# Kernel optimization log

Hardware: AMD Instinct MI355X
Metric: run time of the kernel (lower is better)

The kernel has to match this reference:

```python
import jax, jax.numpy as jnp
import numpy as np

N_E = 4096
E_DIM = 64
BETA = 0.25


def setup_inputs() -> dict:
    key = jax.random.key(0)
    k1, k2 = jax.random.split(key)
    z = jax.random.normal(k1, (16, E_DIM, 32, 32), dtype=jnp.float32)
    embedding = jax.random.normal(k2, (N_E, E_DIM), dtype=jnp.float32)
    return {"z": z, "embedding": embedding}


def reference(z, embedding):
    # b c h w -> b h w c
    zc = jnp.transpose(z, (0, 2, 3, 1))  # [B,H,W,C]
    B, H, W, C = zc.shape
    zf = zc.reshape(-1, C)  # [N, C]

    # Squared Euclidean distances (argmin is identical to cdist p=2 argmin)
    # d2[n,e] = |z|^2 - 2 z.e + |e|^2
    d2 = (
        jnp.sum(zf * zf, axis=1, keepdims=True)
        - 2.0 * (zf @ embedding.T)
        + jnp.sum(embedding * embedding, axis=1)[None, :]
    )  # [N, n_e]
    idx = jnp.argmin(d2, axis=1)  # [N]

    z_q = embedding[idx].reshape(B, H, W, C)

    # dist_p == 2 losses
    loss_d1 = jnp.mean((jax.lax.stop_gradient(z_q) - zc) ** 2)
    loss_d2 = jnp.mean((z_q - jax.lax.stop_gradient(zc)) ** 2)
    loss = BETA * loss_d1 + loss_d2

    # Straight-through estimator
    z_q = zc + jax.lax.stop_gradient(z_q - zc)

    indices = idx.reshape(B, H, W)
    z_q = jnp.transpose(z_q, (0, 3, 1, 2))  # b h w c -> b c h w
    return z_q, loss, indices
```

## Files before the change

kernel.cpp:

```cpp
#include <hip/hip_runtime.h>

typedef float f32x4 __attribute__((ext_vector_type(4)));
typedef short bf16x8 __attribute__((ext_vector_type(8)));

#define HW_ 1024
#define NE_ 4096
#define CHW_ 65536
#define ZQ_SIZE 1048576
#define LOSS_OFF ZQ_SIZE
#define IDX_OFF (ZQ_SIZE + 1)
#define LOSS_SCALE (1.25f / 1048576.f)
#define EPS_GAP 0.1f

union FragU { unsigned u[4]; bf16x8 v; };

__device__ __forceinline__ unsigned umin_(unsigned a, unsigned b) { return a < b ? a : b; }
__device__ __forceinline__ unsigned umax_(unsigned a, unsigned b) { return a > b ? a : b; }

__device__ __forceinline__ void top2_(unsigned key, unsigned& s1, unsigned& s2) {
    unsigned t;
    asm("v_med3_u32 %0, %1, %2, %3" : "=v"(t) : "v"(key), "v"(s1), "v"(s2));
    s2 = t;
    s1 = umin_(s1, key);
}

__device__ __forceinline__ void split8(const float* v, FragU& hi, FragU& lo) {
#pragma unroll
    for (int p = 0; p < 4; p++) {
        float a = v[2 * p], b = v[2 * p + 1];
        unsigned ua = __float_as_uint(a), ub = __float_as_uint(b);
        hi.u[p] = (ua >> 16) | (ub & 0xFFFF0000u);
        float la = a - __uint_as_float(ua & 0xFFFF0000u);
        float lb = b - __uint_as_float(ub & 0xFFFF0000u);
        lo.u[p] = (__float_as_uint(la) >> 16) | (__float_as_uint(lb) & 0xFFFF0000u);
    }
}

__device__ __forceinline__ void gload_lds16(const void* g, void* l) {
    __builtin_amdgcn_global_load_lds(
        (const __attribute__((address_space(1))) unsigned*)g,
        (__attribute__((address_space(3))) unsigned*)l, 16, 0, 0);
}

__global__ __launch_bounds__(256) void vq_pre(
        const float* __restrict__ z, const float* __restrict__ emb,
        float* __restrict__ h_e, float* __restrict__ h_z,
        char* __restrict__ zfrag, char* __restrict__ efrag,
        float* __restrict__ out) {
    const int bid = blockIdx.x, tid = threadIdx.x;
    if (bid < 512) {
        __shared__ float red[2][2][16];
        int u = bid * 256 + tid;
        int l = u & 63, s = (u >> 6) & 1, t = u >> 7;
        int n = t * 16 + (l & 15);
        int b = n >> 10, hw = n & 1023;
        int c0 = s * 32 + (l >> 4) * 8;
        const float* zp = z + (size_t)b * CHW_ + hw;
        float v[8];
        float ss = 0.f;
#pragma unroll
        for (int j = 0; j < 8; j++) {
            v[j] = zp[(c0 + j) * HW_];
            ss = fmaf(v[j], v[j], ss);
        }
        FragU hi, lo;
        split8(v, hi, lo);
        char* base = zfrag + (size_t)t * 4096 + l * 16;
        *(FragU*)(base + s * 1024) = hi;
        *(FragU*)(base + (2 + s) * 1024) = lo;
        ss += __shfl_xor(ss, 16);
        ss += __shfl_xor(ss, 32);
        if ((l >> 4) == 0) red[tid >> 7][s][l & 15] = ss;
        __syncthreads();
        if (tid < 32) {
            int tt = tid >> 4, r = tid & 15;
            h_z[(bid * 2 + tt) * 16 + r] = 0.5f * (red[tt][0][r] + red[tt][1][r]);
        }
    } else if (bid < 640) {
        int u = (bid - 512) * 256 + tid;
        int l = u & 63, s = (u >> 6) & 1, t = u >> 7;
        int er = t * 16 + (l & 15);
        int c0 = s * 32 + (l >> 4) * 8;
        const float* ep = emb + (size_t)er * 64 + c0;
        float4 ea = *(const float4*)(ep);
        float4 eb = *(const float4*)(ep + 4);
        float v[8];
        v[0] = -ea.x; v[1] = -ea.y; v[2] = -ea.z; v[3] = -ea.w;
        v[4] = -eb.x; v[5] = -eb.y; v[6] = -eb.z; v[7] = -eb.w;
        FragU hi, lo;
        split8(v, hi, lo);
        char* base = efrag + (size_t)t * 4096 + l * 16;
        *(FragU*)(base + s * 1024) = hi;
        *(FragU*)(base + (2 + s) * 1024) = lo;
    } else {
        int t = (bid - 640) * 256 + tid;
        const float4* er = (const float4*)(emb + (size_t)t * 64);
        float s = 0.f;
#pragma unroll
        for (int k = 0; k < 16; k++) {
            float4 e4 = er[k];
            s = fmaf(e4.x, e4.x, s); s = fmaf(e4.y, e4.y, s);
            s = fmaf(e4.z, e4.z, s); s = fmaf(e4.w, e4.w, s);
        }
        h_e[t] = 0.5f * s;
        if (t == 0) out[LOSS_OFF] = 0.f;
    }
}

__global__ __launch_bounds__(512) void vq_mfma(
        const char* __restrict__ zfrag, const char* __restrict__ efrag,
        const float* __restrict__ h_e, const float* __restrict__ h_z,
        unsigned* __restrict__ k1q, unsigned* __restrict__ k2q) {
    __shared__ char buf[2][32768];
    __shared__ __attribute__((aligned(16))) float sh_he[512];

    const int tid = threadIdx.x;
    const int lane = tid & 63;
    const int w = tid >> 6;
    const int lrow = lane & 15;
    const int lgrp = lane >> 4;
    const int es = blockIdx.x >> 5;
    const int rb = blockIdx.x & 31;
    const int e0t = es * 32;
    const int rt0 = rb * 32 + w * 4;

    sh_he[tid] = h_e[es * 512 + tid];

    {
        const char* src = efrag + (size_t)(e0t + w) * 4096 + lane * 16;
        char* dst = buf[0] + w * 4096;
#pragma unroll
        for (int i = 0; i < 4; i++) gload_lds16(src + i * 1024, dst + i * 1024);
    }

    bf16x8 zh[4][2], zl[4][2];
    float hz[4];
#pragma unroll
    for (int r = 0; r < 4; r++) {
        const char* zb = zfrag + (size_t)(rt0 + r) * 4096 + lane * 16;
        zh[r][0] = *(const bf16x8*)(zb);
        zh[r][1] = *(const bf16x8*)(zb + 1024);
        zl[r][0] = *(const bf16x8*)(zb + 2048);
        zl[r][1] = *(const bf16x8*)(zb + 3072);
        hz[r] = h_z[(rt0 + r) * 16 + lrow];
    }

    unsigned s1k[4] = {~0u, ~0u, ~0u, ~0u};
    unsigned s2k[4] = {~0u, ~0u, ~0u, ~0u};

    __syncthreads();
    for (int c = 0; c < 4; c++) {
        if (c < 3) {
            const char* src = efrag + (size_t)(e0t + (c + 1) * 8 + w) * 4096
                              + lane * 16;
            char* dst = buf[(c + 1) & 1] + w * 4096;
#pragma unroll
            for (int i = 0; i < 4; i++) gload_lds16(src + i * 1024, dst + i * 1024);
        }

        const char* cb = buf[c & 1] + lane * 16;
#pragma unroll
        for (int j = 0; j < 8; j++) {
            const char* tb = cb + j * 4096;
            bf16x8 ah0 = *(const bf16x8*)(tb);
            bf16x8 ah1 = *(const bf16x8*)(tb + 1024);
            bf16x8 al0 = *(const bf16x8*)(tb + 2048);
            bf16x8 al1 = *(const bf16x8*)(tb + 3072);
            const int etl = c * 8 + j;
            const f32x4 he = *(const f32x4*)&sh_he[etl * 16 + lgrp * 4];

            f32x4 a0 = he + hz[0], a1 = he + hz[1];
            f32x4 a2 = he + hz[2], a3 = he + hz[3];

            a0 = __builtin_amdgcn_mfma_f32_16x16x32_bf16(ah0, zh[0][0], a0, 0, 0, 0);
            a1 = __builtin_amdgcn_mfma_f32_16x16x32_bf16(ah0, zh[1][0], a1, 0, 0, 0);
            a2 = __builtin_amdgcn_mfma_f32_16x16x32_bf16(ah0, zh[2][0], a2, 0, 0, 0);
            a3 = __builtin_amdgcn_mfma_f32_16x16x32_bf16(ah0, zh[3][0], a3, 0, 0, 0);
            a0 = __builtin_amdgcn_mfma_f32_16x16x32_bf16(ah1, zh[0][1], a0, 0, 0, 0);
            a1 = __builtin_amdgcn_mfma_f32_16x16x32_bf16(ah1, zh[1][1], a1, 0, 0, 0);
            a2 = __builtin_amdgcn_mfma_f32_16x16x32_bf16(ah1, zh[2][1], a2, 0, 0, 0);
            a3 = __builtin_amdgcn_mfma_f32_16x16x32_bf16(ah1, zh[3][1], a3, 0, 0, 0);
            a0 = __builtin_amdgcn_mfma_f32_16x16x32_bf16(al0, zh[0][0], a0, 0, 0, 0);
            a1 = __builtin_amdgcn_mfma_f32_16x16x32_bf16(al0, zh[1][0], a1, 0, 0, 0);
            a2 = __builtin_amdgcn_mfma_f32_16x16x32_bf16(al0, zh[2][0], a2, 0, 0, 0);
            a3 = __builtin_amdgcn_mfma_f32_16x16x32_bf16(al0, zh[3][0], a3, 0, 0, 0);
            a0 = __builtin_amdgcn_mfma_f32_16x16x32_bf16(al1, zh[0][1], a0, 0, 0, 0);
            a1 = __builtin_amdgcn_mfma_f32_16x16x32_bf16(al1, zh[1][1], a1, 0, 0, 0);
            a2 = __builtin_amdgcn_mfma_f32_16x16x32_bf16(al1, zh[2][1], a2, 0, 0, 0);
            a3 = __builtin_amdgcn_mfma_f32_16x16x32_bf16(al1, zh[3][1], a3, 0, 0, 0);
            a0 = __builtin_amdgcn_mfma_f32_16x16x32_bf16(ah0, zl[0][0], a0, 0, 0, 0);
            a1 = __builtin_amdgcn_mfma_f32_16x16x32_bf16(ah0, zl[1][0], a1, 0, 0, 0);
            a2 = __builtin_amdgcn_mfma_f32_16x16x32_bf16(ah0, zl[2][0], a2, 0, 0, 0);
            a3 = __builtin_amdgcn_mfma_f32_16x16x32_bf16(ah0, zl[3][0], a3, 0, 0, 0);
            a0 = __builtin_amdgcn_mfma_f32_16x16x32_bf16(ah1, zl[0][1], a0, 0, 0, 0);
            a1 = __builtin_amdgcn_mfma_f32_16x16x32_bf16(ah1, zl[1][1], a1, 0, 0, 0);
            a2 = __builtin_amdgcn_mfma_f32_16x16x32_bf16(ah1, zl[2][1], a2, 0, 0, 0);
            a3 = __builtin_amdgcn_mfma_f32_16x16x32_bf16(ah1, zl[3][1], a3, 0, 0, 0);

            const unsigned eb12 = (unsigned)(es * 512 + etl * 16 + lgrp * 4);
#pragma unroll
            for (int rr = 0; rr < 4; rr++) {
                top2_((__float_as_uint(a0[rr]) & 0xFFFFF000u) | (eb12 + rr), s1k[0], s2k[0]);
                top2_((__float_as_uint(a1[rr]) & 0xFFFFF000u) | (eb12 + rr), s1k[1], s2k[1]);
                top2_((__float_as_uint(a2[rr]) & 0xFFFFF000u) | (eb12 + rr), s1k[2], s2k[2]);
                top2_((__float_as_uint(a3[rr]) & 0xFFFFF000u) | (eb12 + rr), s1k[3], s2k[3]);
            }
        }
        __syncthreads();
    }

#pragma unroll
    for (int off = 16; off <= 32; off += 16) {
#pragma unroll
        for (int r = 0; r < 4; r++) {
            unsigned o1 = (unsigned)__shfl_xor((int)s1k[r], off);
            unsigned o2 = (unsigned)__shfl_xor((int)s2k[r], off);
            s2k[r] = umin_(umin_(s2k[r], o2), umax_(s1k[r], o1));
            s1k[r] = umin_(s1k[r], o1);
        }
    }

    if (lane < 16) {
        const int base = es * 16384;
#pragma unroll
        for (int r = 0; r < 4; r++) {
            k1q[base + (rt0 + r) * 16 + lane] = s1k[r];
            k2q[base + (rt0 + r) * 16 + lane] = s2k[r];
        }
    }
}

__global__ __launch_bounds__(256) void vq_final(
        const float* __restrict__ z, const float* __restrict__ emb,
        const unsigned* __restrict__ k1q, const unsigned* __restrict__ k2q,
        float* __restrict__ out) {
    int t = blockIdx.x * 256 + threadIdx.x;
    int n = t & 16383;
    int q = t >> 14;

    unsigned m = 0xFFFFFFFFu, s = 0xFFFFFFFFu;
#pragma unroll
    for (int i = 0; i < 8; i++) {
        unsigned a = k1q[i * 16384 + n];
        unsigned b = k2q[i * 16384 + n];
        unsigned hi = umax_(m, a);
        m = umin_(m, a);
        s = umin_(umin_(s, b), hi);
    }

    int idx = (int)(m & 0xFFFu);
    float s1 = __uint_as_float(m & 0xFFFFF000u);
    float s2 = __uint_as_float(s & 0xFFFFF000u);

    int b = n >> 10, hw = n & 1023;
    const float* zp = z + (size_t)b * CHW_ + hw;
    const int cq = q * 16;

    if (s2 - s1 < EPS_GAP) {
        int i2 = (int)(s & 0xFFFu);
        const float* ea = emb + (size_t)idx * 64;
        const float* eb = emb + (size_t)i2 * 64;
        double da = 0.0, db = 0.0;
#pragma unroll 8
        for (int c = 0; c < 64; c++) {
            double zv = (double)zp[c * HW_];
            double xa = (double)ea[c] - zv;
            double xb = (double)eb[c] - zv;
            da = fma(xa, xa, da);
            db = fma(xb, xb, db);
        }
        if (db < da || (db == da && i2 < idx)) idx = i2;
    }

    const float* er = emb + (size_t)idx * 64 + cq;
    float* zq = out + (size_t)b * CHW_ + hw;
    float lsum = 0.f;
#pragma unroll
    for (int j = 0; j < 16; j++) {
        float e = er[j];
        float d = e - zp[(cq + j) * HW_];
        zq[(cq + j) * HW_] = e;
        lsum = fmaf(d, d, lsum);
    }
    if (q == 0) out[IDX_OFF + n] = (float)idx;

#pragma unroll
    for (int off = 32; off; off >>= 1) lsum += __shfl_down(lsum, off);
    if ((threadIdx.x & 63) == 0) atomicAdd(&out[LOSS_OFF], lsum * LOSS_SCALE);
}

extern "C" void kernel_launch(void* const* d_in, const int* in_sizes, int n_in,
                              void* d_out, int out_size, void* d_ws, size_t ws_size,
                              hipStream_t stream) {
    const float* z   = (const float*)d_in[0];
    const float* emb = (const float*)d_in[1];
    float* out = (float*)d_out;
    char* ws = (char*)d_ws;

    char* efrag   = ws;
    char* zfrag   = ws + 1048576;
    float* h_e    = (float*)(ws + 5242880);
    float* h_z    = (float*)(ws + 5259264);
    unsigned* k1q = (unsigned*)(ws + 5324800);
    unsigned* k2q = (unsigned*)(ws + 5849088);

    vq_pre  <<<656, 256, 0, stream>>>(z, emb, h_e, h_z, zfrag, efrag, out);
    vq_mfma <<<256, 512, 0, stream>>>(zfrag, efrag, h_e, h_z, k1q, k2q);
    vq_final<<<256, 256, 0, stream>>>(z, emb, k1q, k2q, out);
}
```

Baseline: 51.56 us.

## Fuse z fragment preparation into the MFMA distance kernel

Each MFMA block now loads its z rows directly from the NCHW input, splits them into bf16 hi/lo fragments and computes half the squared norm in registers. This removes the 512 z-preprocessing blocks and the 4 MB zfrag/h_z round trip through global memory, leaving a smaller embedding-only prep kernel. In exchange, each z row is reloaded and re-split by every one of the 8 embedding-slice blocks that share it, using strided channel loads inside the main kernel.

```diff
diff --git a/kernel.cpp b/kernel.cpp
--- a/kernel.cpp
+++ b/kernel.cpp
@@ -42,42 +42,12 @@
         (__attribute__((address_space(3))) unsigned*)l, 16, 0, 0);
 }
 
-__global__ __launch_bounds__(256) void vq_pre(
-        const float* __restrict__ z, const float* __restrict__ emb,
-        float* __restrict__ h_e, float* __restrict__ h_z,
-        char* __restrict__ zfrag, char* __restrict__ efrag,
-        float* __restrict__ out) {
+__global__ __launch_bounds__(256) void vq_eprep(
+        const float* __restrict__ emb, char* __restrict__ efrag,
+        float* __restrict__ h_e, float* __restrict__ out) {
     const int bid = blockIdx.x, tid = threadIdx.x;
-    if (bid < 512) {
-        __shared__ float red[2][2][16];
+    if (bid < 128) {
         int u = bid * 256 + tid;
-        int l = u & 63, s = (u >> 6) & 1, t = u >> 7;
-        int n = t * 16 + (l & 15);
-        int b = n >> 10, hw = n & 1023;
-        int c0 = s * 32 + (l >> 4) * 8;
-        const float* zp = z + (size_t)b * CHW_ + hw;
-        float v[8];
-        float ss = 0.f;
-#pragma unroll
-        for (int j = 0; j < 8; j++) {
-            v[j] = zp[(c0 + j) * HW_];
-            ss = fmaf(v[j], v[j], ss);
-        }
-        FragU hi, lo;
-        split8(v, hi, lo);
-        char* base = zfrag + (size_t)t * 4096 + l * 16;
-        *(FragU*)(base + s * 1024) = hi;
-        *(FragU*)(base + (2 + s) * 1024) = lo;
-        ss += __shfl_xor(ss, 16);
-        ss += __shfl_xor(ss, 32);
-        if ((l >> 4) == 0) red[tid >> 7][s][l & 15] = ss;
-        __syncthreads();
-        if (tid < 32) {
-            int tt = tid >> 4, r = tid & 15;
-            h_z[(bid * 2 + tt) * 16 + r] = 0.5f * (red[tt][0][r] + red[tt][1][r]);
-        }
-    } else if (bid < 640) {
-        int u = (bid - 512) * 256 + tid;
         int l = u & 63, s = (u >> 6) & 1, t = u >> 7;
         int er = t * 16 + (l & 15);
         int c0 = s * 32 + (l >> 4) * 8;
@@ -93,7 +63,7 @@
         *(FragU*)(base + s * 1024) = hi;
         *(FragU*)(base + (2 + s) * 1024) = lo;
     } else {
-        int t = (bid - 640) * 256 + tid;
+        int t = (bid - 128) * 256 + tid;
         const float4* er = (const float4*)(emb + (size_t)t * 64);
         float s = 0.f;
 #pragma unroll
@@ -108,8 +78,8 @@
 }
 
 __global__ __launch_bounds__(512) void vq_mfma(
-        const char* __restrict__ zfrag, const char* __restrict__ efrag,
-        const float* __restrict__ h_e, const float* __restrict__ h_z,
+        const float* __restrict__ z, const char* __restrict__ efrag,
+        const float* __restrict__ h_e,
         unsigned* __restrict__ k1q, unsigned* __restrict__ k2q) {
     __shared__ char buf[2][32768];
     __shared__ __attribute__((aligned(16))) float sh_he[512];
@@ -123,6 +93,7 @@
     const int rb = blockIdx.x & 31;
     const int e0t = es * 32;
     const int rt0 = rb * 32 + w * 4;
+    const int b = rb >> 1;
 
     sh_he[tid] = h_e[es * 512 + tid];
 
@@ -137,12 +108,26 @@
     float hz[4];
 #pragma unroll
     for (int r = 0; r < 4; r++) {
-        const char* zb = zfrag + (size_t)(rt0 + r) * 4096 + lane * 16;
-        zh[r][0] = *(const bf16x8*)(zb);
-        zh[r][1] = *(const bf16x8*)(zb + 1024);
-        zl[r][0] = *(const bf16x8*)(zb + 2048);
-        zl[r][1] = *(const bf16x8*)(zb + 3072);
-        hz[r] = h_z[(rt0 + r) * 16 + lrow];
+        float ss = 0.f;
+#pragma unroll
+        for (int s = 0; s < 2; s++) {
+            const int hw = ((rt0 + r) * 16 + lrow) & 1023;
+            const int c0 = s * 32 + lgrp * 8;
+            const float* zp = z + (size_t)b * CHW_ + hw;
+            float v[8];
+#pragma unroll
+            for (int j = 0; j < 8; j++) {
+                v[j] = zp[(c0 + j) * HW_];
+                ss = fmaf(v[j], v[j], ss);
+            }
+            FragU hi, lo;
+            split8(v, hi, lo);
+            zh[r][s] = hi.v;
+            zl[r][s] = lo.v;
+        }
+        ss += __shfl_xor(ss, 16);
+        ss += __shfl_xor(ss, 32);
+        hz[r] = 0.5f * ss;
     }
 
     unsigned s1k[4] = {~0u, ~0u, ~0u, ~0u};
@@ -298,13 +283,11 @@
     char* ws = (char*)d_ws;
 
     char* efrag   = ws;
-    char* zfrag   = ws + 1048576;
-    float* h_e    = (float*)(ws + 5242880);
-    float* h_z    = (float*)(ws + 5259264);
-    unsigned* k1q = (unsigned*)(ws + 5324800);
-    unsigned* k2q = (unsigned*)(ws + 5849088);
-
-    vq_pre  <<<656, 256, 0, stream>>>(z, emb, h_e, h_z, zfrag, efrag, out);
-    vq_mfma <<<256, 512, 0, stream>>>(zfrag, efrag, h_e, h_z, k1q, k2q);
+    float* h_e    = (float*)(ws + 1048576);
+    unsigned* k1q = (unsigned*)(ws + 1065024);
+    unsigned* k2q = (unsigned*)(ws + 1589312);
+
+    vq_eprep<<<144, 256, 0, stream>>>(emb, efrag, h_e, out);
+    vq_mfma <<<256, 512, 0, stream>>>(z, efrag, h_e, k1q, k2q);
     vq_final<<<256, 256, 0, stream>>>(z, emb, k1q, k2q, out);
 }
```

Measured after the change: 51.55 us. No clear change (-0.0%).
